# Kernel optimization log

Hardware: AMD Instinct MI355X
Metric: run time of the kernel (lower is better)

## Reference

```python
import jax, jax.numpy as jnp
import numpy as np

B, R, SR, K, F = 1, 4096, 40, 8, 32
H = 256           # shading_feature_num
NVF = 4           # num_viewdir_freqs -> 2*4*3 = 24 PE channels
EPS = 1e-8


def positional_encoding(x, n_freqs):
    # x: [..., 3] -> [..., 2*n_freqs*3]
    freqs = (2.0 ** jnp.arange(n_freqs)).astype(x.dtype)          # [nf]
    ang = x[..., None, :] * freqs[:, None]                        # [..., nf, 3]
    enc = jnp.concatenate([jnp.sin(ang), jnp.cos(ang)], axis=-1)  # [..., nf, 6]
    return enc.reshape(x.shape[:-1] + (2 * n_freqs * 3,))


def setup_inputs() -> dict:
    key = jax.random.key(0)
    ks = jax.random.split(key, 20)
    s = 0.02
    inp = {
        "sampled_embedding": jax.random.normal(ks[0], (B, R, SR, K, F), jnp.float32),
        "dists": jax.random.normal(ks[1], (B, R, SR, K, 3), jnp.float32),
        "viewdirs": jax.random.normal(ks[2], (B, R, SR, 3), jnp.float32),
        "pnt_mask": jax.random.randint(ks[3], (B, R, SR, K), 0, 2, jnp.int32),
        # block1: Linear(F,H), Linear(H,H)
        "W1a": jax.random.normal(ks[4], (F, H), jnp.float32) * s,
        "b1a": jnp.zeros((H,), jnp.float32),
        "W1b": jax.random.normal(ks[5], (H, H), jnp.float32) * s,
        "b1b": jnp.zeros((H,), jnp.float32),
        # block3: Linear(H,H), Linear(H,H)
        "W3a": jax.random.normal(ks[6], (H, H), jnp.float32) * s,
        "b3a": jnp.zeros((H,), jnp.float32),
        "W3b": jax.random.normal(ks[7], (H, H), jnp.float32) * s,
        "b3b": jnp.zeros((H,), jnp.float32),
        # alpha branch: Linear(H,1)
        "Wa": jax.random.normal(ks[8], (H, 1), jnp.float32) * s,
        "ba": jnp.zeros((1,), jnp.float32),
        # color branch: Linear(H + 24, 3)
        "Wc": jax.random.normal(ks[9], (H + 2 * NVF * 3, 3), jnp.float32) * s,
        "bc": jnp.zeros((3,), jnp.float32),
    }
    return inp


def reference(sampled_embedding, dists, viewdirs, pnt_mask,
              W1a, b1a, W1b, b1b, W3a, b3a, W3b, b3b, Wa, ba, Wc, bc):
    mask = pnt_mask.astype(sampled_embedding.dtype)               # [B,R,SR,K]
    # quadric distance kernel: w = mask / max(||d||^2, eps)
    d2 = jnp.sum(dists * dists, axis=-1)                          # [B,R,SR,K]
    w = mask / jnp.maximum(d2, EPS)
    # agg_weight_norm: normalize over neighbors
    w = w / jnp.maximum(jnp.sum(w, axis=-1, keepdims=True), EPS)
    # agg_intrp_order == 0: interpolate features first
    feat = jnp.einsum('brsk,brskf->brsf', w, sampled_embedding)   # [B,R,SR,F]
    h = jax.nn.relu(feat @ W1a + b1a)
    h = jax.nn.relu(h @ W1b + b1b)
    h = jax.nn.relu(h @ W3a + b3a)
    h = jax.nn.relu(h @ W3b + b3b)
    # alpha branch + raw2out_density (act_super=1 -> softplus(x-1))
    alpha = jax.nn.softplus(h @ Wa + ba - 1.0)                    # [B,R,SR,1]
    # color branch: concat viewdir PE, then raw2out_color
    vd = viewdirs / jnp.maximum(jnp.linalg.norm(viewdirs, axis=-1, keepdims=True), EPS)
    vpe = positional_encoding(vd, NVF)                            # [B,R,SR,24]
    raw_c = jnp.concatenate([h, vpe], axis=-1) @ Wc + bc          # [B,R,SR,3]
    color = jax.nn.sigmoid(raw_c) * (1.0 + 2e-3) - 1e-3
    return jnp.concatenate([alpha, color], axis=-1)               # [B,R,SR,4]
```

## Files before the change

kernel.cpp:

```cpp
#include <hip/hip_runtime.h>
#include <hip/hip_bf16.h>
#include <cstdint>

typedef __attribute__((ext_vector_type(8))) short short8;
typedef __attribute__((ext_vector_type(4))) float floatx4;
typedef __attribute__((ext_vector_type(4))) float fx4;

#define ROWS 128
#define NTHREADS 256
#define RSTRIDE 296

#define BAR_PLAIN asm volatile("s_barrier" ::: "memory")
#define BAR_LGKM  asm volatile("s_waitcnt lgkmcnt(0)\n\ts_barrier" ::: "memory")

__device__ __forceinline__ ushort f2bf(float x) {
  union { float f; uint32_t u; } v; v.f = x;
  uint32_t r = v.u + 0x7fffu + ((v.u >> 16) & 1u);
  return (ushort)(r >> 16);
}

__device__ __forceinline__ uint32_t cvtpk2(float lo, float hi) {
  uint32_t r;
  asm("v_cvt_pk_bf16_f32 %0, %1, %2" : "=v"(r) : "v"(lo), "v"(hi));
  return r;
}

__global__ void prep_kernel(const float* __restrict__ W1a, const float* __restrict__ W1b,
                            const float* __restrict__ W3a, const float* __restrict__ W3b,
                            const float* __restrict__ Wa,  const float* __restrict__ Wc,
                            const float* __restrict__ ba,  const float* __restrict__ bc,
                            ushort* __restrict__ W1aT, ushort* __restrict__ W1bT,
                            ushort* __restrict__ W3aT, ushort* __restrict__ W3bT,
                            ushort* __restrict__ whead, float* __restrict__ hbias)
{
  int b = blockIdx.x, t = threadIdx.x;
  W1bT[t * 256 + b] = f2bf(W1b[b * 256 + t]);
  W3aT[t * 256 + b] = f2bf(W3a[b * 256 + t]);
  W3bT[t * 256 + b] = f2bf(W3b[b * 256 + t]);
  if (b < 32) W1aT[t * 32 + b] = f2bf(W1a[b * 256 + t]);
  if (b == 255) {
    for (int k = t; k < 288; k += 256) {
      for (int r = 0; r < 16; ++r) {
        float v = 0.f;
        if (r == 0)     v = (k < 256) ? Wa[k] : 0.f;
        else if (r < 4) v = (k < 280) ? Wc[k * 3 + (r - 1)] : 0.f;
        whead[r * 288 + k] = f2bf(v);
      }
    }
    if (t == 0) { hbias[0] = ba[0]; hbias[1] = bc[0]; hbias[2] = bc[1]; hbias[3] = bc[2]; }
  }
}

template<int NKT, int KST>
__device__ __forceinline__ void mlp_layer(ushort (*buf)[RSTRIDE],
                                          const ushort* __restrict__ WT,
                                          const float* __restrict__ bias,
                                          int mbase, int lrow, int kgrp)
{
  floatx4 acc[4][8] = {};
  short8 a[4];
  #pragma unroll
  for (int mt = 0; mt < 4; ++mt)
    a[mt] = *(const short8*)&WT[(size_t)(mbase + mt * 16 + lrow) * KST + kgrp * 8];
  __builtin_amdgcn_s_setprio(1);
  #pragma unroll
  for (int kt = 0; kt < NKT; ++kt) {
    short8 an[4];
    if (kt + 1 < NKT) {
      #pragma unroll
      for (int mt = 0; mt < 4; ++mt)
        an[mt] = *(const short8*)&WT[(size_t)(mbase + mt * 16 + lrow) * KST
                                     + (kt + 1) * 32 + kgrp * 8];
    }
    short8 b[8];
    #pragma unroll
    for (int nt = 0; nt < 8; ++nt)
      b[nt] = *(const short8*)&buf[nt * 16 + lrow][kt * 32 + kgrp * 8];
    #pragma unroll
    for (int mt = 0; mt < 4; ++mt)
      #pragma unroll
      for (int nt = 0; nt < 8; ++nt)
        acc[mt][nt] = __builtin_amdgcn_mfma_f32_16x16x32_bf16(a[mt], b[nt], acc[mt][nt], 0, 0, 0);
    if (kt + 1 < NKT) {
      #pragma unroll
      for (int mt = 0; mt < 4; ++mt) a[mt] = an[mt];
    }
  }
  __builtin_amdgcn_s_setprio(0);
  BAR_PLAIN;
  #pragma unroll
  for (int mt = 0; mt < 4; ++mt) {
    float4 bv = *(const float4*)(bias + mbase + mt * 16 + kgrp * 4);
    #pragma unroll
    for (int nt = 0; nt < 8; ++nt) {
      uint2 pk;
      pk.x = cvtpk2(fmaxf(acc[mt][nt][0] + bv.x, 0.f), fmaxf(acc[mt][nt][1] + bv.y, 0.f));
      pk.y = cvtpk2(fmaxf(acc[mt][nt][2] + bv.z, 0.f), fmaxf(acc[mt][nt][3] + bv.w, 0.f));
      *(uint2*)&buf[nt * 16 + lrow][mbase + mt * 16 + kgrp * 4] = pk;
    }
  }
  BAR_LGKM;
}

__global__ __launch_bounds__(NTHREADS, 2) void pa_fused(
    const float* __restrict__ emb, const float* __restrict__ dists,
    const float* __restrict__ viewdirs, const int* __restrict__ pnt_mask,
    const ushort* __restrict__ W1aT, const float* __restrict__ b1a,
    const ushort* __restrict__ W1bT, const float* __restrict__ b1b,
    const ushort* __restrict__ W3aT, const float* __restrict__ b3a,
    const ushort* __restrict__ W3bT, const float* __restrict__ b3b,
    const ushort* __restrict__ whead, const float* __restrict__ hbias,
    float* __restrict__ out)
{
  __shared__ ushort buf[ROWS][RSTRIDE];
  const int tid  = threadIdx.x;
  const int base = blockIdx.x * ROWS;

  {
    const int s = tid >> 1, g = tid & 1;
    const int gs = base + s;
    float d[24];
    const float4* d4 = (const float4*)(dists + (size_t)gs * 24);
    #pragma unroll
    for (int i = 0; i < 6; ++i) {
      float4 q = d4[i];
      d[4*i] = q.x; d[4*i+1] = q.y; d[4*i+2] = q.z; d[4*i+3] = q.w;
    }
    const int4* m4 = (const int4*)(pnt_mask + (size_t)gs * 8);
    int4 m0 = m4[0], m1 = m4[1];
    int mk[8] = {m0.x, m0.y, m0.z, m0.w, m1.x, m1.y, m1.z, m1.w};
    float wv[8]; float sum = 0.f;
    #pragma unroll
    for (int k = 0; k < 8; ++k) {
      float d2 = d[3*k]*d[3*k] + d[3*k+1]*d[3*k+1] + d[3*k+2]*d[3*k+2];
      wv[k] = (float)mk[k] * __builtin_amdgcn_rcpf(fmaxf(d2, 1e-8f));
      sum += wv[k];
    }
    float inv = __builtin_amdgcn_rcpf(fmaxf(sum, 1e-8f));
    #pragma unroll
    for (int k = 0; k < 8; ++k) wv[k] *= inv;

    float acc[16];
    #pragma unroll
    for (int j = 0; j < 16; ++j) acc[j] = 0.f;
    #pragma unroll
    for (int k = 0; k < 8; ++k) {
      const fx4* e4 = (const fx4*)(emb + ((size_t)(gs * 8 + k)) * 32 + g * 16);
      fx4 e0 = __builtin_nontemporal_load(e4);
      fx4 e1 = __builtin_nontemporal_load(e4 + 1);
      fx4 e2 = __builtin_nontemporal_load(e4 + 2);
      fx4 e3 = __builtin_nontemporal_load(e4 + 3);
      acc[0]  += wv[k]*e0.x; acc[1]  += wv[k]*e0.y; acc[2]  += wv[k]*e0.z; acc[3]  += wv[k]*e0.w;
      acc[4]  += wv[k]*e1.x; acc[5]  += wv[k]*e1.y; acc[6]  += wv[k]*e1.z; acc[7]  += wv[k]*e1.w;
      acc[8]  += wv[k]*e2.x; acc[9]  += wv[k]*e2.y; acc[10] += wv[k]*e2.z; acc[11] += wv[k]*e2.w;
      acc[12] += wv[k]*e3.x; acc[13] += wv[k]*e3.y; acc[14] += wv[k]*e3.z; acc[15] += wv[k]*e3.w;
    }
    uint4 fp0, fp1;
    fp0.x = cvtpk2(acc[0],  acc[1]);  fp0.y = cvtpk2(acc[2],  acc[3]);
    fp0.z = cvtpk2(acc[4],  acc[5]);  fp0.w = cvtpk2(acc[6],  acc[7]);
    fp1.x = cvtpk2(acc[8],  acc[9]);  fp1.y = cvtpk2(acc[10], acc[11]);
    fp1.z = cvtpk2(acc[12], acc[13]); fp1.w = cvtpk2(acc[14], acc[15]);
    *(uint4*)&buf[s][g * 16]     = fp0;
    *(uint4*)&buf[s][g * 16 + 8] = fp1;

    float vx = viewdirs[(size_t)gs * 3 + 0];
    float vy = viewdirs[(size_t)gs * 3 + 1];
    float vz = viewdirs[(size_t)gs * 3 + 2];
    float nrm = sqrtf(vx*vx + vy*vy + vz*vz);
    float ninv = __builtin_amdgcn_rcpf(fmaxf(nrm, 1e-8f));
    uint32_t* pe = (uint32_t*)&buf[s][256 + g * 12];
    #pragma unroll
    for (int h = 0; h < 2; ++h) {
      float fr = (float)(1 << (2 * g + h)) * ninv;
      float sx, cx, sy, cy, sz, cz;
      sincosf(vx * fr, &sx, &cx);
      sincosf(vy * fr, &sy, &cy);
      sincosf(vz * fr, &sz, &cz);
      pe[3*h + 0] = cvtpk2(sx, sy);
      pe[3*h + 1] = cvtpk2(sz, cx);
      pe[3*h + 2] = cvtpk2(cy, cz);
    }
    if (g == 1) {
      uint4 z = {0, 0, 0, 0};
      *(uint4*)&buf[s][280] = z;
    }
  }
  BAR_LGKM;

  const int lane = tid & 63;
  const int wid  = tid >> 6;
  const int lrow = lane & 15;
  const int kgrp = lane >> 4;
  const int mbase = wid * 64;

  mlp_layer<1, 32>(buf, W1aT, b1a, mbase, lrow, kgrp);
  mlp_layer<8, 256>(buf, W1bT, b1b, mbase, lrow, kgrp);
  mlp_layer<8, 256>(buf, W3aT, b3a, mbase, lrow, kgrp);
  mlp_layer<8, 256>(buf, W3bT, b3b, mbase, lrow, kgrp);

  #pragma unroll
  for (int h = 0; h < 2; ++h) {
    floatx4 hacc = {0.f, 0.f, 0.f, 0.f};
    #pragma unroll
    for (int kt = 0; kt < 9; ++kt) {
      short8 a = *(const short8*)&whead[(size_t)lrow * 288 + kt * 32 + kgrp * 8];
      short8 b = *(const short8*)&buf[wid * 32 + h * 16 + lrow][kt * 32 + kgrp * 8];
      hacc = __builtin_amdgcn_mfma_f32_16x16x32_bf16(a, b, hacc, 0, 0, 0);
    }
    if (lane < 16) {
      float4 hb = *(const float4*)hbias;
      float ra = hacc[0] + hb.x - 1.f;
      float alpha = fmaxf(ra, 0.f) + log1pf(expf(-fabsf(ra)));
      float c0 = hacc[1] + hb.y, c1 = hacc[2] + hb.z, c2 = hacc[3] + hb.w;
      fx4 o;
      o.x = alpha;
      o.y = 1.f / (1.f + expf(-c0)) * 1.002f - 1e-3f;
      o.z = 1.f / (1.f + expf(-c1)) * 1.002f - 1e-3f;
      o.w = 1.f / (1.f + expf(-c2)) * 1.002f - 1e-3f;
      int gs = base + wid * 32 + h * 16 + lane;
      __builtin_nontemporal_store(o, (fx4*)(out + (size_t)gs * 4));
    }
  }
}

extern "C" void kernel_launch(void* const* d_in, const int* in_sizes, int n_in,
                              void* d_out, int out_size, void* d_ws, size_t ws_size,
                              hipStream_t stream)
{
  const float* emb   = (const float*)d_in[0];
  const float* dists = (const float*)d_in[1];
  const float* vdirs = (const float*)d_in[2];
  const int*   mask  = (const int*)d_in[3];
  const float* W1a = (const float*)d_in[4];
  const float* b1a = (const float*)d_in[5];
  const float* W1b = (const float*)d_in[6];
  const float* b1b = (const float*)d_in[7];
  const float* W3a = (const float*)d_in[8];
  const float* b3a = (const float*)d_in[9];
  const float* W3b = (const float*)d_in[10];
  const float* b3b = (const float*)d_in[11];
  const float* Wa  = (const float*)d_in[12];
  const float* ba  = (const float*)d_in[13];
  const float* Wc  = (const float*)d_in[14];
  const float* bc  = (const float*)d_in[15];

  ushort* wsb  = (ushort*)d_ws;
  ushort* W1aT  = wsb;
  ushort* W1bT  = wsb + 8192;
  ushort* W3aT  = wsb + 73728;
  ushort* W3bT  = wsb + 139264;
  ushort* whead = wsb + 204800;
  float*  hbias = (float*)(wsb + 209408);

  prep_kernel<<<256, 256, 0, stream>>>(W1a, W1b, W3a, W3b, Wa, Wc, ba, bc,
                                       W1aT, W1bT, W3aT, W3bT, whead, hbias);

  int nsamples = in_sizes[2] / 3;
  int nblocks  = nsamples / ROWS;
  pa_fused<<<nblocks, NTHREADS, 0, stream>>>(emb, dists, vdirs, mask,
                                             W1aT, b1a, W1bT, b1b, W3aT, b3a, W3bT, b3b,
                                             whead, hbias, (float*)d_out);
}
```

Measured before the change: 129.7 us.

## Split gather/aggregate phase into separate kernel writing bf16 features to workspace

Splits the fused kernel into two. A lightweight aggregation kernel computes the weighted neighbor features and the viewdir encoding and stores them as bf16 in workspace, then an MLP kernel loads them into LDS and runs the MFMA layers. The goal is to separate the memory-bound gather from the LDS-heavy MLP so each kernel runs at its own best occupancy, instead of MLP blocks stalling on global loads. The cost is an extra launch and a round trip of the intermediate through global memory. A fused fallback is kept for when the workspace is too small.

```diff
diff --git a/kernel.cpp b/kernel.cpp
--- a/kernel.cpp
+++ b/kernel.cpp
@@ -5,6 +5,7 @@
 typedef __attribute__((ext_vector_type(8))) short short8;
 typedef __attribute__((ext_vector_type(4))) float floatx4;
 typedef __attribute__((ext_vector_type(4))) float fx4;
+typedef __attribute__((ext_vector_type(4))) uint ux4;
 
 #define ROWS 128
 #define NTHREADS 256
@@ -51,6 +52,89 @@
   }
 }
 
+__device__ __forceinline__ void phaseA_compute(
+    const float* __restrict__ emb, const float* __restrict__ dists,
+    const float* __restrict__ viewdirs, const int* __restrict__ pnt_mask,
+    int gs, int g, ux4& u0, ux4& u1, ux4& u2, ux4& u3)
+{
+  float d[24];
+  const float4* d4 = (const float4*)(dists + (size_t)gs * 24);
+  #pragma unroll
+  for (int i = 0; i < 6; ++i) {
+    float4 q = d4[i];
+    d[4*i] = q.x; d[4*i+1] = q.y; d[4*i+2] = q.z; d[4*i+3] = q.w;
+  }
+  const int4* m4 = (const int4*)(pnt_mask + (size_t)gs * 8);
+  int4 m0 = m4[0], m1 = m4[1];
+  int mk[8] = {m0.x, m0.y, m0.z, m0.w, m1.x, m1.y, m1.z, m1.w};
+  float wv[8]; float sum = 0.f;
+  #pragma unroll
+  for (int k = 0; k < 8; ++k) {
+    float d2 = d[3*k]*d[3*k] + d[3*k+1]*d[3*k+1] + d[3*k+2]*d[3*k+2];
+    wv[k] = (float)mk[k] * __builtin_amdgcn_rcpf(fmaxf(d2, 1e-8f));
+    sum += wv[k];
+  }
+  float inv = __builtin_amdgcn_rcpf(fmaxf(sum, 1e-8f));
+  #pragma unroll
+  for (int k = 0; k < 8; ++k) wv[k] *= inv;
+
+  float acc[16];
+  #pragma unroll
+  for (int j = 0; j < 16; ++j) acc[j] = 0.f;
+  #pragma unroll
+  for (int k = 0; k < 8; ++k) {
+    const fx4* e4 = (const fx4*)(emb + ((size_t)(gs * 8 + k)) * 32 + g * 16);
+    fx4 e0 = __builtin_nontemporal_load(e4);
+    fx4 e1 = __builtin_nontemporal_load(e4 + 1);
+    fx4 e2 = __builtin_nontemporal_load(e4 + 2);
+    fx4 e3 = __builtin_nontemporal_load(e4 + 3);
+    acc[0]  += wv[k]*e0.x; acc[1]  += wv[k]*e0.y; acc[2]  += wv[k]*e0.z; acc[3]  += wv[k]*e0.w;
+    acc[4]  += wv[k]*e1.x; acc[5]  += wv[k]*e1.y; acc[6]  += wv[k]*e1.z; acc[7]  += wv[k]*e1.w;
+    acc[8]  += wv[k]*e2.x; acc[9]  += wv[k]*e2.y; acc[10] += wv[k]*e2.z; acc[11] += wv[k]*e2.w;
+    acc[12] += wv[k]*e3.x; acc[13] += wv[k]*e3.y; acc[14] += wv[k]*e3.z; acc[15] += wv[k]*e3.w;
+  }
+  u0.x = cvtpk2(acc[0],  acc[1]);  u0.y = cvtpk2(acc[2],  acc[3]);
+  u0.z = cvtpk2(acc[4],  acc[5]);  u0.w = cvtpk2(acc[6],  acc[7]);
+  u1.x = cvtpk2(acc[8],  acc[9]);  u1.y = cvtpk2(acc[10], acc[11]);
+  u1.z = cvtpk2(acc[12], acc[13]); u1.w = cvtpk2(acc[14], acc[15]);
+
+  float vx = viewdirs[(size_t)gs * 3 + 0];
+  float vy = viewdirs[(size_t)gs * 3 + 1];
+  float vz = viewdirs[(size_t)gs * 3 + 2];
+  float nrm = sqrtf(vx*vx + vy*vy + vz*vz);
+  float ninv = __builtin_amdgcn_rcpf(fmaxf(nrm, 1e-8f));
+  uint32_t pd[6];
+  #pragma unroll
+  for (int h = 0; h < 2; ++h) {
+    float fr = (float)(1 << (2 * g + h)) * ninv;
+    float sx, cx, sy, cy, sz, cz;
+    sincosf(vx * fr, &sx, &cx);
+    sincosf(vy * fr, &sy, &cy);
+    sincosf(vz * fr, &sz, &cz);
+    pd[3*h + 0] = cvtpk2(sx, sy);
+    pd[3*h + 1] = cvtpk2(sz, cx);
+    pd[3*h + 2] = cvtpk2(cy, cz);
+  }
+  u2.x = pd[0]; u2.y = pd[1]; u2.z = pd[2]; u2.w = pd[3];
+  u3.x = pd[4]; u3.y = pd[5]; u3.z = 0u;    u3.w = 0u;
+}
+
+__global__ __launch_bounds__(256) void k_aggregate(
+    const float* __restrict__ emb, const float* __restrict__ dists,
+    const float* __restrict__ viewdirs, const int* __restrict__ pnt_mask,
+    ushort* __restrict__ featg)
+{
+  int tid = blockIdx.x * 256 + threadIdx.x;
+  int s = tid >> 1, g = tid & 1;
+  ux4 u0, u1, u2, u3;
+  phaseA_compute(emb, dists, viewdirs, pnt_mask, s, g, u0, u1, u2, u3);
+  ux4* dst = (ux4*)(featg + (size_t)s * 64 + g * 32);
+  __builtin_nontemporal_store(u0, dst + 0);
+  __builtin_nontemporal_store(u1, dst + 1);
+  __builtin_nontemporal_store(u2, dst + 2);
+  __builtin_nontemporal_store(u3, dst + 3);
+}
+
 template<int NKT, int KST>
 __device__ __forceinline__ void mlp_layer(ushort (*buf)[RSTRIDE],
                                           const ushort* __restrict__ WT,
@@ -102,9 +186,8 @@
   BAR_LGKM;
 }
 
-__global__ __launch_bounds__(NTHREADS, 2) void pa_fused(
-    const float* __restrict__ emb, const float* __restrict__ dists,
-    const float* __restrict__ viewdirs, const int* __restrict__ pnt_mask,
+__device__ __forceinline__ void mlp_and_head(
+    ushort (*buf)[RSTRIDE], int tid, int base,
     const ushort* __restrict__ W1aT, const float* __restrict__ b1a,
     const ushort* __restrict__ W1bT, const float* __restrict__ b1b,
     const ushort* __restrict__ W3aT, const float* __restrict__ b3a,
@@ -112,81 +195,6 @@
     const ushort* __restrict__ whead, const float* __restrict__ hbias,
     float* __restrict__ out)
 {
-  __shared__ ushort buf[ROWS][RSTRIDE];
-  const int tid  = threadIdx.x;
-  const int base = blockIdx.x * ROWS;
-
-  {
-    const int s = tid >> 1, g = tid & 1;
-    const int gs = base + s;
-    float d[24];
-    const float4* d4 = (const float4*)(dists + (size_t)gs * 24);
-    #pragma unroll
-    for (int i = 0; i < 6; ++i) {
-      float4 q = d4[i];
-      d[4*i] = q.x; d[4*i+1] = q.y; d[4*i+2] = q.z; d[4*i+3] = q.w;
-    }
-    const int4* m4 = (const int4*)(pnt_mask + (size_t)gs * 8);
-    int4 m0 = m4[0], m1 = m4[1];
-    int mk[8] = {m0.x, m0.y, m0.z, m0.w, m1.x, m1.y, m1.z, m1.w};
-    float wv[8]; float sum = 0.f;
-    #pragma unroll
-    for (int k = 0; k < 8; ++k) {
-      float d2 = d[3*k]*d[3*k] + d[3*k+1]*d[3*k+1] + d[3*k+2]*d[3*k+2];
-      wv[k] = (float)mk[k] * __builtin_amdgcn_rcpf(fmaxf(d2, 1e-8f));
-      sum += wv[k];
-    }
-    float inv = __builtin_amdgcn_rcpf(fmaxf(sum, 1e-8f));
-    #pragma unroll
-    for (int k = 0; k < 8; ++k) wv[k] *= inv;
-
-    float acc[16];
-    #pragma unroll
-    for (int j = 0; j < 16; ++j) acc[j] = 0.f;
-    #pragma unroll
-    for (int k = 0; k < 8; ++k) {
-      const fx4* e4 = (const fx4*)(emb + ((size_t)(gs * 8 + k)) * 32 + g * 16);
-      fx4 e0 = __builtin_nontemporal_load(e4);
-      fx4 e1 = __builtin_nontemporal_load(e4 + 1);
-      fx4 e2 = __builtin_nontemporal_load(e4 + 2);
-      fx4 e3 = __builtin_nontemporal_load(e4 + 3);
-      acc[0]  += wv[k]*e0.x; acc[1]  += wv[k]*e0.y; acc[2]  += wv[k]*e0.z; acc[3]  += wv[k]*e0.w;
-      acc[4]  += wv[k]*e1.x; acc[5]  += wv[k]*e1.y; acc[6]  += wv[k]*e1.z; acc[7]  += wv[k]*e1.w;
-      acc[8]  += wv[k]*e2.x; acc[9]  += wv[k]*e2.y; acc[10] += wv[k]*e2.z; acc[11] += wv[k]*e2.w;
-      acc[12] += wv[k]*e3.x; acc[13] += wv[k]*e3.y; acc[14] += wv[k]*e3.z; acc[15] += wv[k]*e3.w;
-    }
-    uint4 fp0, fp1;
-    fp0.x = cvtpk2(acc[0],  acc[1]);  fp0.y = cvtpk2(acc[2],  acc[3]);
-    fp0.z = cvtpk2(acc[4],  acc[5]);  fp0.w = cvtpk2(acc[6],  acc[7]);
-    fp1.x = cvtpk2(acc[8],  acc[9]);  fp1.y = cvtpk2(acc[10], acc[11]);
-    fp1.z = cvtpk2(acc[12], acc[13]); fp1.w = cvtpk2(acc[14], acc[15]);
-    *(uint4*)&buf[s][g * 16]     = fp0;
-    *(uint4*)&buf[s][g * 16 + 8] = fp1;
-
-    float vx = viewdirs[(size_t)gs * 3 + 0];
-    float vy = viewdirs[(size_t)gs * 3 + 1];
-    float vz = viewdirs[(size_t)gs * 3 + 2];
-    float nrm = sqrtf(vx*vx + vy*vy + vz*vz);
-    float ninv = __builtin_amdgcn_rcpf(fmaxf(nrm, 1e-8f));
-    uint32_t* pe = (uint32_t*)&buf[s][256 + g * 12];
-    #pragma unroll
-    for (int h = 0; h < 2; ++h) {
-      float fr = (float)(1 << (2 * g + h)) * ninv;
-      float sx, cx, sy, cy, sz, cz;
-      sincosf(vx * fr, &sx, &cx);
-      sincosf(vy * fr, &sy, &cy);
-      sincosf(vz * fr, &sz, &cz);
-      pe[3*h + 0] = cvtpk2(sx, sy);
-      pe[3*h + 1] = cvtpk2(sz, cx);
-      pe[3*h + 2] = cvtpk2(cy, cz);
-    }
-    if (g == 1) {
-      uint4 z = {0, 0, 0, 0};
-      *(uint4*)&buf[s][280] = z;
-    }
-  }
-  BAR_LGKM;
-
   const int lane = tid & 63;
   const int wid  = tid >> 6;
   const int lrow = lane & 15;
@@ -221,6 +229,73 @@
       __builtin_nontemporal_store(o, (fx4*)(out + (size_t)gs * 4));
     }
   }
+}
+
+__global__ __launch_bounds__(NTHREADS, 2) void k_mlp(
+    const ushort* __restrict__ featg,
+    const ushort* __restrict__ W1aT, const float* __restrict__ b1a,
+    const ushort* __restrict__ W1bT, const float* __restrict__ b1b,
+    const ushort* __restrict__ W3aT, const float* __restrict__ b3a,
+    const ushort* __restrict__ W3bT, const float* __restrict__ b3b,
+    const ushort* __restrict__ whead, const float* __restrict__ hbias,
+    float* __restrict__ out)
+{
+  __shared__ ushort buf[ROWS][RSTRIDE];
+  const int tid  = threadIdx.x;
+  const int base = blockIdx.x * ROWS;
+
+  {
+    const int s = tid >> 1, g = tid & 1;
+    const ux4* src = (const ux4*)(featg + (size_t)(base + s) * 64 + g * 32);
+    ux4 u0 = src[0], u1 = src[1], u2 = src[2], u3 = src[3];
+    *(ux4*)&buf[s][g * 16]     = u0;
+    *(ux4*)&buf[s][g * 16 + 8] = u1;
+    uint2* pe = (uint2*)&buf[s][256 + g * 12];
+    pe[0] = make_uint2(u2.x, u2.y);
+    pe[1] = make_uint2(u2.z, u2.w);
+    pe[2] = make_uint2(u3.x, u3.y);
+    if (g == 1) {
+      ux4 z = {0, 0, 0, 0};
+      *(ux4*)&buf[s][280] = z;
+    }
+  }
+  BAR_LGKM;
+
+  mlp_and_head(buf, tid, base, W1aT, b1a, W1bT, b1b, W3aT, b3a, W3bT, b3b,
+               whead, hbias, out);
+}
+
+__global__ __launch_bounds__(NTHREADS, 2) void pa_fused_fb(
+    const float* __restrict__ emb, const float* __restrict__ dists,
+    const float* __restrict__ viewdirs, const int* __restrict__ pnt_mask,
+    const ushort* __restrict__ W1aT, const float* __restrict__ b1a,
+    const ushort* __restrict__ W1bT, const float* __restrict__ b1b,
+    const ushort* __restrict__ W3aT, const float* __restrict__ b3a,
+    const ushort* __restrict__ W3bT, const float* __restrict__ b3b,
+    const ushort* __restrict__ whead, const float* __restrict__ hbias,
+    float* __restrict__ out)
+{
+  __shared__ ushort buf[ROWS][RSTRIDE];
+  const int tid  = threadIdx.x;
+  const int base = blockIdx.x * ROWS;
+  {
+    const int s = tid >> 1, g = tid & 1;
+    ux4 u0, u1, u2, u3;
+    phaseA_compute(emb, dists, viewdirs, pnt_mask, base + s, g, u0, u1, u2, u3);
+    *(ux4*)&buf[s][g * 16]     = u0;
+    *(ux4*)&buf[s][g * 16 + 8] = u1;
+    uint2* pe = (uint2*)&buf[s][256 + g * 12];
+    pe[0] = make_uint2(u2.x, u2.y);
+    pe[1] = make_uint2(u2.z, u2.w);
+    pe[2] = make_uint2(u3.x, u3.y);
+    if (g == 1) {
+      ux4 z = {0, 0, 0, 0};
+      *(ux4*)&buf[s][280] = z;
+    }
+  }
+  BAR_LGKM;
+  mlp_and_head(buf, tid, base, W1aT, b1a, W1bT, b1b, W3aT, b3a, W3bT, b3b,
+               whead, hbias, out);
 }
 
 extern "C" void kernel_launch(void* const* d_in, const int* in_sizes, int n_in,
@@ -244,6 +319,8 @@
   const float* Wc  = (const float*)d_in[14];
   const float* bc  = (const float*)d_in[15];
 
+  int nsamples = in_sizes[2] / 3;
+
   ushort* wsb  = (ushort*)d_ws;
   ushort* W1aT  = wsb;
   ushort* W1bT  = wsb + 8192;
@@ -251,13 +328,21 @@
   ushort* W3bT  = wsb + 139264;
   ushort* whead = wsb + 204800;
   float*  hbias = (float*)(wsb + 209408);
+  ushort* featg = wsb + 209424;
+  size_t ws_needed = ((size_t)209424 + (size_t)nsamples * 64) * 2;
 
   prep_kernel<<<256, 256, 0, stream>>>(W1a, W1b, W3a, W3b, Wa, Wc, ba, bc,
                                        W1aT, W1bT, W3aT, W3bT, whead, hbias);
 
-  int nsamples = in_sizes[2] / 3;
-  int nblocks  = nsamples / ROWS;
-  pa_fused<<<nblocks, NTHREADS, 0, stream>>>(emb, dists, vdirs, mask,
-                                             W1aT, b1a, W1bT, b1b, W3aT, b3a, W3bT, b3b,
-                                             whead, hbias, (float*)d_out);
-}
+  int nblocks = nsamples / ROWS;
+  if (ws_size >= ws_needed) {
+    k_aggregate<<<nsamples * 2 / 256, 256, 0, stream>>>(emb, dists, vdirs, mask, featg);
+    k_mlp<<<nblocks, NTHREADS, 0, stream>>>(featg,
+                                            W1aT, b1a, W1bT, b1b, W3aT, b3a, W3bT, b3b,
+                                            whead, hbias, (float*)d_out);
+  } else {
+    pa_fused_fb<<<nblocks, NTHREADS, 0, stream>>>(emb, dists, vdirs, mask,
+                                                  W1aT, b1a, W1bT, b1b, W3aT, b3a, W3bT, b3b,
+                                                  whead, hbias, (float*)d_out);
+  }
+}
```

Result: slower. 155.2 us (+19.6%).
